# Performance work log

Measured on AMD Instinct MI355X. Metric: run time of the kernel, lower is better.

## Reference

```python
import jax, jax.numpy as jnp
import numpy as np

B = 32
IMG = 512
P = 32            # patch_size (must equal 32 so bounding_box Linear(32,4) type-checks)
G = IMG // P      # 16
N = G * G         # 256 num_patches
PD = P * P * 3    # 3072 patch_dim
D = 512           # project_dim
H = 8             # num_heads
DH = D // H
L = 4             # transformer blocks
HEAD_DIMS = [N * D, 2048, 1024, 512, 64, 32]
EPS = 1e-6


def _mk(key, shape, scale=0.02):
    return (jax.random.normal(key, shape, dtype=jnp.float32) * scale)


def setup_inputs() -> dict:
    key = jax.random.key(0)
    ks = jax.random.split(key, 32)
    inp = {"images": jax.random.normal(ks[0], (B, IMG, IMG, 3), dtype=jnp.float32)}
    # patch encoder
    inp["W_proj"] = _mk(ks[1], (PD, D))
    inp["b_proj"] = jnp.zeros((D,), jnp.float32)
    inp["pos_emb"] = _mk(ks[2], (N, D))
    # stacked transformer block params [L, ...]
    inp["ln1_g"] = jnp.ones((L, D), jnp.float32)
    inp["ln1_b"] = jnp.zeros((L, D), jnp.float32)
    inp["qkv_w"] = _mk(ks[3], (L, 3 * D, D))
    inp["qkv_b"] = jnp.zeros((L, 3 * D), jnp.float32)
    inp["attn_out_w"] = _mk(ks[4], (L, D, D))
    inp["attn_out_b"] = jnp.zeros((L, D), jnp.float32)
    inp["ln2_g"] = jnp.ones((L, D), jnp.float32)
    inp["ln2_b"] = jnp.zeros((L, D), jnp.float32)
    inp["mlp_w1"] = _mk(ks[5], (L, D, 2 * D))
    inp["mlp_b1"] = jnp.zeros((L, 2 * D), jnp.float32)
    inp["mlp_w2"] = _mk(ks[6], (L, 2 * D, D))
    inp["mlp_b2"] = jnp.zeros((L, D), jnp.float32)
    # final LN
    inp["lnf_g"] = jnp.ones((D,), jnp.float32)
    inp["lnf_b"] = jnp.zeros((D,), jnp.float32)
    # MLP head (5 layers) + bbox
    for i in range(5):
        inp[f"hW{i+1}"] = _mk(ks[7 + i], (HEAD_DIMS[i], HEAD_DIMS[i + 1]))
        inp[f"hb{i+1}"] = jnp.zeros((HEAD_DIMS[i + 1],), jnp.float32)
    inp["bbW"] = _mk(ks[20], (32, 4))
    inp["bbb"] = jnp.zeros((4,), jnp.float32)
    return inp


def _ln(x, g, b):
    m = jnp.mean(x, axis=-1, keepdims=True)
    v = jnp.mean((x - m) ** 2, axis=-1, keepdims=True)
    return (x - m) * jax.lax.rsqrt(v + EPS) * g + b


def _patches(images):
    # fused unfold: [B,IMG,IMG,3] -> [B,N,P*P*3], flatten order (ph, pw, c)
    x = images.reshape(B, G, P, G, P, 3)
    x = x.transpose(0, 1, 3, 2, 4, 5)  # [B,G,G,P,P,3]
    return x.reshape(B, N, PD)


def _block(x, ln1_g, ln1_b, qkv_w, qkv_b, out_w, out_b, ln2_g, ln2_b, w1, b1, w2, b2):
    x1 = _ln(x, ln1_g, ln1_b)
    qkv = x1 @ qkv_w.T + qkv_b  # [B,N,3D]
    q, k, v = jnp.split(qkv, 3, axis=-1)
    q = q.reshape(B, N, H, DH).transpose(0, 2, 1, 3)
    k = k.reshape(B, N, H, DH).transpose(0, 2, 1, 3)
    v = v.reshape(B, N, H, DH).transpose(0, 2, 1, 3)
    scores = jnp.einsum("bhqd,bhkd->bhqk", q, k) / jnp.sqrt(jnp.float32(DH))
    attn = jax.nn.softmax(scores, axis=-1)
    o = jnp.einsum("bhqk,bhkd->bhqd", attn, v)
    o = o.transpose(0, 2, 1, 3).reshape(B, N, D)
    attn_out = o @ out_w.T + out_b
    x2 = attn_out + x
    x3 = _ln(x2, ln2_g, ln2_b)
    h = jax.nn.gelu(x3 @ w1 + b1, approximate=False)
    h = jax.nn.gelu(h @ w2 + b2, approximate=False)
    return h + x2


def reference(images, W_proj, b_proj, pos_emb,
              ln1_g, ln1_b, qkv_w, qkv_b, attn_out_w, attn_out_b,
              ln2_g, ln2_b, mlp_w1, mlp_b1, mlp_w2, mlp_b2,
              lnf_g, lnf_b,
              hW1, hb1, hW2, hb2, hW3, hb3, hW4, hb4, hW5, hb5,
              bbW, bbb):
    patches = _patches(images)                       # [B,N,PD]
    x = patches @ W_proj + b_proj + pos_emb          # [B,N,D]
    for i in range(L):
        x = _block(x, ln1_g[i], ln1_b[i], qkv_w[i], qkv_b[i],
                   attn_out_w[i], attn_out_b[i], ln2_g[i], ln2_b[i],
                   mlp_w1[i], mlp_b1[i], mlp_w2[i], mlp_b2[i])
    rep = _ln(x, lnf_g, lnf_b).reshape(B, N * D)
    f = rep
    for (w, b) in [(hW1, hb1), (hW2, hb2), (hW3, hb3), (hW4, hb4), (hW5, hb5)]:
        f = jax.nn.gelu(f @ w + b, approximate=False)
    return f @ bbW + bbb                              # [B,4]
```

## Files before the change

kernel.cpp:

```cpp
#include <hip/hip_runtime.h>
#include <cstdint>
#include <cstddef>

#define DEV __device__ __forceinline__

typedef float f32x4 __attribute__((ext_vector_type(4)));
typedef short s16x8 __attribute__((ext_vector_type(8)));

DEV float gelu_f(float x) { return 0.5f * x * (1.0f + erff(x * 0.70710678118654752f)); }

DEV uint32_t fbits(float x) { return __builtin_bit_cast(uint32_t, x); }

DEV uint16_t bf16_rne(float x) {
    uint32_t u = fbits(x);
    return (uint16_t)((u + 0x7FFFu + ((u >> 16) & 1u)) >> 16);
}

DEV void gload16(const void* g, void* l) {
    __builtin_amdgcn_global_load_lds(
        (const __attribute__((address_space(1))) uint32_t*)g,
        (__attribute__((address_space(3))) uint32_t*)l, 16, 0, 0);
}

template<int BM, int BN, bool BIAS, bool GELU, bool RES, bool POS,
         bool OUTF32, bool OUTB16>
__global__ __launch_bounds__(256)
void mfma_gemm(const uint16_t* __restrict__ Ah, const uint16_t* __restrict__ Bh,
               float* __restrict__ C, uint16_t* __restrict__ Cb,
               const float* __restrict__ bias, const float* __restrict__ res,
               const float* __restrict__ pos, int M, int N, int K)
{
    constexpr int WTM = BM / 2, WTN = BN / 2;
    constexpr int FM = WTM / 16, FN = WTN / 16;
    constexpr int NA = BM / 16, NB = BN / 16;
    constexpr int TI = NA + NB;
    constexpr int TI4 = TI / 4;
    constexpr int HALF = (BM + BN) * 64;
    constexpr int BNP = BN + 4;
    constexpr int CR  = 32;
    constexpr int NCH = BM / CR;
    static_assert(CR * BNP * 4 <= 2 * HALF, "chunk must fit LDS");

    __shared__ __align__(16) uint8_t smem[2 * HALF];
    constexpr int offB = BM * 64;

    const int tid = threadIdx.x;
    const int w = tid >> 6, l = tid & 63;
    const int wr = w >> 1, wc = w & 1;

    const int gx = gridDim.x;
    const int nwg = gx * gridDim.y;
    const int lin = blockIdx.y * gx + blockIdx.x;
    const int cpx = nwg >> 3;
    const int swz = (lin & 7) * cpx + (lin >> 3);
    const int bxs = swz % gx, bys = swz / gx;
    const int bm0 = bys * BM, bn0 = bxs * BN;
    const size_t sK = (size_t)K * 2;

    const int srow  = l >> 2;
    const int sslot = (l & 3) ^ ((l >> 3) & 3);
    const uint8_t* gsrc[TI4];
    uint32_t loff[TI4];
#pragma unroll
    for (int j = 0; j < TI4; ++j) {
        int f = w * TI4 + j;
        int p = (f < NA) ? 0 : 1;
        int c = p ? (f - NA) : f;
        const uint16_t* base = p ? Bh : Ah;
        int rb = p ? bn0 : bm0;
        gsrc[j] = (const uint8_t*)base + (size_t)(rb + c * 16 + srow) * sK + sslot * 16;
        loff[j] = (uint32_t)((p ? offB : 0) + c * 1024);
    }

    const int lr = l & 15;
    const int sl16 = ((l >> 4) ^ ((lr >> 1) & 3)) * 16;
    const int aofs = (wr * WTM + lr) * 64 + sl16;
    const int bofs = (wc * WTN + lr) * 64 + sl16;

    f32x4 acc[FM][FN];
#pragma unroll
    for (int m = 0; m < FM; ++m)
#pragma unroll
        for (int n = 0; n < FN; ++n) acc[m][n] = (f32x4){0.f, 0.f, 0.f, 0.f};

    {
        const uint8_t* s0 = smem;
#pragma unroll
        for (int j = 0; j < TI4; ++j)
            gload16(gsrc[j], (void*)(s0 + loff[j]));
    }
    asm volatile("s_waitcnt vmcnt(0)" ::: "memory");
    __builtin_amdgcn_s_barrier();

    int cur = 0;
    for (int k0 = 0; k0 < K; k0 += 32) {
        const bool more = (k0 + 32 < K);
        if (more) {
            const size_t kb = (size_t)(k0 + 32) * 2;
            uint8_t* dst = smem + (cur ^ 1) * HALF;
#pragma unroll
            for (int j = 0; j < TI4; ++j)
                gload16(gsrc[j] + kb, dst + loff[j]);
        }
        const uint8_t* sb = smem + cur * HALF;
        s16x8 af[FM], bf[FN];
#pragma unroll
        for (int m = 0; m < FM; ++m)
            af[m] = *(const s16x8*)(sb + aofs + m * 1024);
#pragma unroll
        for (int n = 0; n < FN; ++n)
            bf[n] = *(const s16x8*)(sb + offB + bofs + n * 1024);
#pragma unroll
        for (int m = 0; m < FM; ++m)
#pragma unroll
            for (int n = 0; n < FN; ++n)
                acc[m][n] = __builtin_amdgcn_mfma_f32_16x16x32_bf16(af[m], bf[n], acc[m][n], 0, 0, 0);

        if (more) {
            asm volatile("s_waitcnt vmcnt(0)" ::: "memory");
            __builtin_amdgcn_s_barrier();
        }
        cur ^= 1;
    }

    float* lf = (float*)smem;
    const int r4 = (l >> 4) * 4;

    constexpr int C4PR = BN / 4;
    constexpr int RPP  = 256 / C4PR;
    const int rr = tid / C4PR, c4 = tid % C4PR;
    const int nn = bn0 + c4 * 4;

    float4 bv = {0.f, 0.f, 0.f, 0.f};
    if (BIAS) bv = *(const float4*)(bias + nn);

#pragma unroll
    for (int c = 0; c < NCH; ++c) {
        __syncthreads();
        if (wr == (c * CR) / WTM) {
            const int mlo = ((c * CR) % WTM) / 16;
#pragma unroll
            for (int mi = 0; mi < CR / 16; ++mi) {
                int m = mlo + mi;
#pragma unroll
                for (int n = 0; n < FN; ++n) {
                    int col = wc * WTN + n * 16 + lr;
#pragma unroll
                    for (int r = 0; r < 4; ++r) {
                        int lrow = mi * 16 + r4 + r;
                        lf[lrow * BNP + col] = acc[m][n][r];
                    }
                }
            }
        }
        __syncthreads();
#pragma unroll
        for (int p = 0; p < CR / RPP; ++p) {
            int row = p * RPP + rr;
            int mm = bm0 + c * CR + row;
            float4 v = *(const float4*)&lf[row * BNP + c4 * 4];
            float* vp = &v.x;
            const float* bp = &bv.x;
#pragma unroll
            for (int q = 0; q < 4; ++q) {
                float x = vp[q];
                if (BIAS) x += bp[q];
                if (GELU) x = gelu_f(x);
                vp[q] = x;
            }
            if (RES) {
                float4 rv = *(const float4*)(res + (size_t)mm * N + nn);
                v.x += rv.x; v.y += rv.y; v.z += rv.z; v.w += rv.w;
            }
            if (POS) {
                float4 pv = *(const float4*)(pos + (size_t)(mm & 255) * N + nn);
                v.x += pv.x; v.y += pv.y; v.z += pv.z; v.w += pv.w;
            }
            size_t o = (size_t)mm * N + nn;
            if (OUTF32) *(float4*)(C + o) = v;
            if (OUTB16) {
                ushort4 hh;
                hh.x = bf16_rne(v.x); hh.y = bf16_rne(v.y);
                hh.z = bf16_rne(v.z); hh.w = bf16_rne(v.w);
                *(ushort4*)(Cb + o) = hh;
            }
        }
    }
}

__global__ __launch_bounds__(256)
void mfma_attn(const uint16_t* __restrict__ QKVb, uint16_t* __restrict__ Oh)
{
    __shared__ __align__(16) uint8_t lds[55296];
    uint8_t* Ks = lds;
    uint8_t* Vt = lds + 9216;
    uint8_t* Ps = lds + 18432;

    const int tid = threadIdx.x;
    const int w = tid >> 6, l = tid & 63;
    const int lr = l & 15, lg = l >> 4;
    const int bh = blockIdx.x;
    const int b = bh >> 3, h = bh & 7;
    const uint16_t* base = QKVb + (size_t)b * 256 * 1536 + h * 64;
    const int q0 = w * 64;

    s16x8 qreg[2][4];
#pragma unroll
    for (int ks = 0; ks < 2; ++ks)
#pragma unroll
        for (int m = 0; m < 4; ++m)
            qreg[ks][m] = *(const s16x8*)(base + (size_t)(q0 + m * 16 + lr) * 1536 + ks * 32 + lg * 8);

    f32x4 oacc[4][4];
    float lrun[4][4];
#pragma unroll
    for (int m = 0; m < 4; ++m)
#pragma unroll
        for (int n = 0; n < 4; ++n) { oacc[m][n] = (f32x4){0.f,0.f,0.f,0.f}; lrun[m][n] = 0.f; }

    for (int kt = 0; kt < 4; ++kt) {
        __syncthreads();
        {
            int r = tid >> 2, sp = (tid & 3) * 2;
            const uint16_t* kp = base + (size_t)(kt * 64 + r) * 1536 + 512;
#pragma unroll
            for (int ss = 0; ss < 2; ++ss) {
                int s = sp + ss;
                *(s16x8*)(Ks + r * 144 + s * 16) = *(const s16x8*)(kp + s * 8);
            }
        }
        {
            int k = tid & 63, d0 = (tid >> 6) * 16;
            const uint16_t* vp = base + (size_t)(kt * 64 + k) * 1536 + 1024 + d0;
            s16x8 a = *(const s16x8*)(vp);
            s16x8 c = *(const s16x8*)(vp + 8);
#pragma unroll
            for (int i = 0; i < 8; ++i) {
                *(uint16_t*)(Vt + (d0 + i) * 144 + k * 2)     = (uint16_t)a[i];
                *(uint16_t*)(Vt + (d0 + 8 + i) * 144 + k * 2) = (uint16_t)c[i];
            }
        }
        __syncthreads();

        f32x4 sacc[4][4];
#pragma unroll
        for (int m = 0; m < 4; ++m)
#pragma unroll
            for (int n = 0; n < 4; ++n) sacc[m][n] = (f32x4){0.f,0.f,0.f,0.f};
#pragma unroll
        for (int ks = 0; ks < 2; ++ks) {
            s16x8 kf[4];
#pragma unroll
            for (int n = 0; n < 4; ++n)
                kf[n] = *(const s16x8*)(Ks + (n * 16 + lr) * 144 + ks * 64 + lg * 16);
#pragma unroll
            for (int m = 0; m < 4; ++m)
#pragma unroll
                for (int n = 0; n < 4; ++n)
                    sacc[m][n] = __builtin_amdgcn_mfma_f32_16x16x32_bf16(qreg[ks][m], kf[n], sacc[m][n], 0, 0, 0);
        }

        float dp[4][4];
#pragma unroll
        for (int m = 0; m < 4; ++m)
#pragma unroll
            for (int r = 0; r < 4; ++r) dp[m][r] = 0.f;
#pragma unroll
        for (int m = 0; m < 4; ++m) {
#pragma unroll
            for (int n = 0; n < 4; ++n) {
#pragma unroll
                for (int r = 0; r < 4; ++r) {
                    float e = __expf(sacc[m][n][r] * 0.125f);
                    dp[m][r] += e;
                    int q = q0 + m * 16 + lg * 4 + r;
                    int k = n * 16 + lr;
                    *(uint16_t*)(Ps + q * 144 + k * 2) = bf16_rne(e);
                }
            }
        }
#pragma unroll
        for (int m = 0; m < 4; ++m)
#pragma unroll
            for (int r = 0; r < 4; ++r) {
                float d = dp[m][r];
                d += __shfl_xor(d, 1);
                d += __shfl_xor(d, 2);
                d += __shfl_xor(d, 4);
                d += __shfl_xor(d, 8);
                lrun[m][r] += d;
            }

        asm volatile("s_waitcnt lgkmcnt(0)" ::: "memory");
        __builtin_amdgcn_sched_barrier(0);

#pragma unroll
        for (int ks = 0; ks < 2; ++ks) {
            s16x8 pf[4], vf[4];
#pragma unroll
            for (int m = 0; m < 4; ++m)
                pf[m] = *(const s16x8*)(Ps + (q0 + m * 16 + lr) * 144 + ks * 64 + lg * 16);
#pragma unroll
            for (int n = 0; n < 4; ++n)
                vf[n] = *(const s16x8*)(Vt + (n * 16 + lr) * 144 + ks * 64 + lg * 16);
#pragma unroll
            for (int m = 0; m < 4; ++m)
#pragma unroll
                for (int n = 0; n < 4; ++n)
                    oacc[m][n] = __builtin_amdgcn_mfma_f32_16x16x32_bf16(pf[m], vf[n], oacc[m][n], 0, 0, 0);
        }
    }

    float inv[4][4];
#pragma unroll
    for (int m = 0; m < 4; ++m)
#pragma unroll
        for (int r = 0; r < 4; ++r) inv[m][r] = 1.f / lrun[m][r];

    float* OL = (float*)lds;
#pragma unroll
    for (int c = 0; c < 2; ++c) {
        __syncthreads();
        if ((w >> 1) == c) {
            const int lq0 = q0 - c * 128;
#pragma unroll
            for (int m = 0; m < 4; ++m)
#pragma unroll
                for (int n = 0; n < 4; ++n)
#pragma unroll
                    for (int r = 0; r < 4; ++r) {
                        int lq = lq0 + m * 16 + lg * 4 + r;
                        int d = n * 16 + lr;
                        OL[lq * 68 + d] = oacc[m][n][r] * inv[m][r];
                    }
        }
        __syncthreads();
#pragma unroll
        for (int p = 0; p < 8; ++p) {
            int lq = p * 16 + (tid >> 4);
            int q = c * 128 + lq;
            int d4 = tid & 15;
            f32x4 v = *(const f32x4*)(OL + lq * 68 + d4 * 4);
            ushort4 hh;
            hh.x = bf16_rne(v[0]); hh.y = bf16_rne(v[1]);
            hh.z = bf16_rne(v[2]); hh.w = bf16_rne(v[3]);
            size_t o = (size_t)(b * 256 + q) * 512 + h * 64 + d4 * 4;
            *(ushort4*)(Oh + o) = hh;
        }
    }
}

__global__ __launch_bounds__(256)
void img2planes_kernel(const float* __restrict__ img, uint16_t* __restrict__ Ph)
{
    int idx = blockIdx.x * 256 + threadIdx.x;
    if (idx >= 8192 * 768) return;
    int m = idx / 768, q = idx - (idx / 768) * 768;
    int k = q * 4;
    int bb = m >> 8, n = m & 255;
    int ph = k / 96, rem = k - ph * 96;
    int prow = ((n >> 4) << 5) + ph;
    int pcol0 = (n & 15) << 5;
    const float* s = img + (((size_t)bb * 512 + prow) * 512 + pcol0) * 3 + rem;
    float4 v = *(const float4*)s;
    ushort4 hh;
    hh.x = bf16_rne(v.x); hh.y = bf16_rne(v.y);
    hh.z = bf16_rne(v.z); hh.w = bf16_rne(v.w);
    *(ushort4*)(Ph + (size_t)m * 3072 + k) = hh;
}

__global__ __launch_bounds__(256)
void conv_direct_kernel(const float* __restrict__ src, uint16_t* __restrict__ dh, int total4)
{
    int idx = blockIdx.x * 256 + threadIdx.x;
    if (idx >= total4) return;
    float4 v = *(const float4*)(src + (size_t)idx * 4);
    ushort4 hh;
    hh.x = bf16_rne(v.x); hh.y = bf16_rne(v.y);
    hh.z = bf16_rne(v.z); hh.w = bf16_rne(v.w);
    *(ushort4*)(dh + (size_t)idx * 4) = hh;
}

__global__ __launch_bounds__(256)
void conv_transpose_kernel(const float* __restrict__ src, uint16_t* __restrict__ dh,
                           int K, int N)
{
    __shared__ float t[32][33];
    int k0 = blockIdx.x * 32, n0 = blockIdx.y * 32;
    const float* s = src + (size_t)blockIdx.z * K * N;
    size_t dbase = (size_t)blockIdx.z * N * K;
    int tid = threadIdx.x;
    {
        int kk = tid / 8, n4 = tid % 8;
        float4 v = *(const float4*)(s + (size_t)(k0 + kk) * N + n0 + n4 * 4);
        t[kk][n4 * 4 + 0] = v.x; t[kk][n4 * 4 + 1] = v.y;
        t[kk][n4 * 4 + 2] = v.z; t[kk][n4 * 4 + 3] = v.w;
    }
    __syncthreads();
    int nn = tid / 8, k4 = tid % 8;
    ushort4 hh;
    hh.x = bf16_rne(t[k4 * 4 + 0][nn]);
    hh.y = bf16_rne(t[k4 * 4 + 1][nn]);
    hh.z = bf16_rne(t[k4 * 4 + 2][nn]);
    hh.w = bf16_rne(t[k4 * 4 + 3][nn]);
    *(ushort4*)(dh + dbase + (size_t)(n0 + nn) * K + k0 + k4 * 4) = hh;
}

template<bool PLANES>
__global__ __launch_bounds__(256)
void ln_kernel(const float* __restrict__ X, const float* __restrict__ g,
               const float* __restrict__ b, float* __restrict__ Y,
               uint16_t* __restrict__ Yh, int nrows)
{
    int wave = threadIdx.x >> 6;
    int lane = threadIdx.x & 63;
    int row = blockIdx.x * 4 + wave;
    if (row >= nrows) return;
    const float* x = X + (size_t)row * 512;
    float4 v0 = ((const float4*)x)[lane];
    float4 v1 = ((const float4*)x)[lane + 64];
    float s  = v0.x + v0.y + v0.z + v0.w + v1.x + v1.y + v1.z + v1.w;
    float sq = v0.x*v0.x + v0.y*v0.y + v0.z*v0.z + v0.w*v0.w
             + v1.x*v1.x + v1.y*v1.y + v1.z*v1.z + v1.w*v1.w;
#pragma unroll
    for (int off = 32; off > 0; off >>= 1) {
        s  += __shfl_down(s, off);
        sq += __shfl_down(sq, off);
    }
    s  = __shfl(s, 0);
    sq = __shfl(sq, 0);
    float mean = s * (1.f / 512.f);
    float var  = sq * (1.f / 512.f) - mean * mean;
    float rinv = rsqrtf(var + 1e-6f);
    float4 g0 = ((const float4*)g)[lane], g1 = ((const float4*)g)[lane + 64];
    float4 b0 = ((const float4*)b)[lane], b1 = ((const float4*)b)[lane + 64];
    float4 o0, o1;
    o0.x = (v0.x - mean) * rinv * g0.x + b0.x;
    o0.y = (v0.y - mean) * rinv * g0.y + b0.y;
    o0.z = (v0.z - mean) * rinv * g0.z + b0.z;
    o0.w = (v0.w - mean) * rinv * g0.w + b0.w;
    o1.x = (v1.x - mean) * rinv * g1.x + b1.x;
    o1.y = (v1.y - mean) * rinv * g1.y + b1.y;
    o1.z = (v1.z - mean) * rinv * g1.z + b1.z;
    o1.w = (v1.w - mean) * rinv * g1.w + b1.w;
    if (PLANES) {
        ushort4 hh0, hh1;
        hh0.x = bf16_rne(o0.x); hh0.y = bf16_rne(o0.y);
        hh0.z = bf16_rne(o0.z); hh0.w = bf16_rne(o0.w);
        hh1.x = bf16_rne(o1.x); hh1.y = bf16_rne(o1.y);
        hh1.z = bf16_rne(o1.z); hh1.w = bf16_rne(o1.w);
        size_t base = (size_t)row * 512;
        *(ushort4*)(Yh + base + lane * 4)       = hh0;
        *(ushort4*)(Yh + base + 256 + lane * 4) = hh1;
    } else {
        float* y = Y + (size_t)row * 512;
        ((float4*)y)[lane]      = o0;
        ((float4*)y)[lane + 64] = o1;
    }
}

template<int BM, int BN, int BK, int TM, int TN, bool SPLITK>
__global__ __launch_bounds__(256)
void gemm_kernel(const float* __restrict__ A, const float* __restrict__ B,
                 float* __restrict__ C, int M, int N, int K, int kchunk)
{
    constexpr int TX = BN / TN;
    constexpr int TY = BM / TM;
    static_assert(TX * TY == 256, "bad tile config");
    __shared__ float As[BK][BM + 4];
    __shared__ float Bs[BK][BN + 4];
    const int tid = threadIdx.x;
    const int tx  = tid % TX;
    const int ty  = tid / TX;
    const int bn0 = blockIdx.x * BN;
    const int bm0 = blockIdx.y * BM;
    int kstart = 0, kend = K;
    if (SPLITK) { kstart = blockIdx.z * kchunk; kend = kstart + kchunk; }
    float acc[TM][TN];
#pragma unroll
    for (int i = 0; i < TM; ++i)
#pragma unroll
        for (int j = 0; j < TN; ++j) acc[i][j] = 0.f;
    for (int k0 = kstart; k0 < kend; k0 += BK) {
        __syncthreads();
        constexpr int AV = BM * BK / 4 / 256;
#pragma unroll
        for (int r = 0; r < AV; ++r) {
            int idx = tid + r * 256;
            int k4 = idx % (BK / 4);
            int mm = idx / (BK / 4);
            float4 v = *(const float4*)(A + (size_t)(bm0 + mm) * K + k0 + k4 * 4);
            As[k4 * 4 + 0][mm] = v.x;
            As[k4 * 4 + 1][mm] = v.y;
            As[k4 * 4 + 2][mm] = v.z;
            As[k4 * 4 + 3][mm] = v.w;
        }
        constexpr int BV = BK * BN / 4 / 256;
#pragma unroll
        for (int r = 0; r < BV; ++r) {
            int idx = tid + r * 256;
            int n4 = idx % (BN / 4);
            int kk = idx / (BN / 4);
            float4 v = *(const float4*)(B + (size_t)(k0 + kk) * N + bn0 + n4 * 4);
            *(float4*)&Bs[kk][n4 * 4] = v;
        }
        __syncthreads();
#pragma unroll
        for (int kk = 0; kk < BK; ++kk) {
            float a[TM], b[TN];
#pragma unroll
            for (int i = 0; i < TM; i += 4)
                *(float4*)&a[i] = *(const float4*)&As[kk][ty * TM + i];
#pragma unroll
            for (int j = 0; j < TN; j += 4)
                *(float4*)&b[j] = *(const float4*)&Bs[kk][tx * TN + j];
#pragma unroll
            for (int i = 0; i < TM; ++i)
#pragma unroll
                for (int j = 0; j < TN; ++j)
                    acc[i][j] = fmaf(a[i], b[j], acc[i][j]);
        }
    }
    float* Cb = C;
    if (SPLITK) Cb += (size_t)blockIdx.z * M * N;
#pragma unroll
    for (int i = 0; i < TM; ++i) {
        int m = bm0 + ty * TM + i;
#pragma unroll
        for (int j = 0; j < TN; j += 4) {
            int n = bn0 + tx * TN + j;
            float4 v;
            v.x = acc[i][j + 0]; v.y = acc[i][j + 1];
            v.z = acc[i][j + 2]; v.w = acc[i][j + 3];
            *(float4*)(Cb + (size_t)m * N + n) = v;
        }
    }
}

__global__ __launch_bounds__(256)
void skinny_gemm_kernel(const float* __restrict__ A, const float* __restrict__ B,
                        float* __restrict__ P, int M, int N, int K, int kchunk)
{
    __shared__ float As[32][36];
    const int tid = threadIdx.x;
    const int tx  = tid & 63;
    const int ty  = tid >> 6;
    const int bn0 = blockIdx.x * 64;
    const int kstart = blockIdx.y * kchunk;
    const int kend   = kstart + kchunk;
    float acc[8];
#pragma unroll
    for (int i = 0; i < 8; ++i) acc[i] = 0.f;
    for (int k0 = kstart; k0 < kend; k0 += 32) {
        __syncthreads();
        {
            int row = tid >> 3;
            int k4  = tid & 7;
            float4 v = *(const float4*)(A + (size_t)row * K + k0 + k4 * 4);
            *(float4*)&As[row][k4 * 4] = v;
        }
        __syncthreads();
#pragma unroll 8
        for (int kk = 0; kk < 32; ++kk) {
            float b = B[(size_t)(k0 + kk) * N + bn0 + tx];
#pragma unroll
            for (int i = 0; i < 8; ++i)
                acc[i] = fmaf(As[ty * 8 + i][kk], b, acc[i]);
        }
    }
    float* Pb = P + (size_t)blockIdx.y * M * N;
#pragma unroll
    for (int i = 0; i < 8; ++i)
        Pb[(size_t)(ty * 8 + i) * N + bn0 + tx] = acc[i];
}

__global__ __launch_bounds__(256)
void reduce_gelu_kernel(const float* __restrict__ P, const float* __restrict__ bias,
                        float* __restrict__ Y, int total, int chunks, int N)
{
    int idx = blockIdx.x * 256 + threadIdx.x;
    if (idx >= total) return;
    float s = 0.f;
    for (int c = 0; c < chunks; ++c) s += P[(size_t)c * total + idx];
    s += bias[idx % N];
    Y[idx] = gelu_f(s);
}

template<bool GELU>
__global__ __launch_bounds__(256)
void small_gemm_kernel(const float* __restrict__ A, const float* __restrict__ B,
                       const float* __restrict__ bias, float* __restrict__ C,
                       int M, int N, int K)
{
    int idx = blockIdx.x * 256 + threadIdx.x;
    if (idx >= M * N) return;
    int m = idx / N, n = idx % N;
    const float* a = A + (size_t)m * K;
    float s = 0.f;
    for (int k = 0; k < K; ++k) s = fmaf(a[k], B[(size_t)k * N + n], s);
    s += bias[n];
    if (GELU) s = gelu_f(s);
    C[idx] = s;
}

extern "C" void kernel_launch(void* const* d_in, const int* in_sizes, int n_in,
                              void* d_out, int out_size, void* d_ws, size_t ws_size,
                              hipStream_t stream)
{
    const float* images     = (const float*)d_in[0];
    const float* W_proj     = (const float*)d_in[1];
    const float* b_proj     = (const float*)d_in[2];
    const float* pos_emb    = (const float*)d_in[3];
    const float* ln1_g      = (const float*)d_in[4];
    const float* ln1_b      = (const float*)d_in[5];
    const float* qkv_w      = (const float*)d_in[6];
    const float* qkv_b      = (const float*)d_in[7];
    const float* attn_out_w = (const float*)d_in[8];
    const float* attn_out_b = (const float*)d_in[9];
    const float* ln2_g      = (const float*)d_in[10];
    const float* ln2_b      = (const float*)d_in[11];
    const float* mlp_w1     = (const float*)d_in[12];
    const float* mlp_b1     = (const float*)d_in[13];
    const float* mlp_w2     = (const float*)d_in[14];
    const float* mlp_b2     = (const float*)d_in[15];
    const float* lnf_g      = (const float*)d_in[16];
    const float* lnf_b      = (const float*)d_in[17];
    const float* hW1 = (const float*)d_in[18];
    const float* hb1 = (const float*)d_in[19];
    const float* hW2 = (const float*)d_in[20];
    const float* hb2 = (const float*)d_in[21];
    const float* hW3 = (const float*)d_in[22];
    const float* hb3 = (const float*)d_in[23];
    const float* hW4 = (const float*)d_in[24];
    const float* hb4 = (const float*)d_in[25];
    const float* hW5 = (const float*)d_in[26];
    const float* hb5 = (const float*)d_in[27];
    const float* bbW = (const float*)d_in[28];
    const float* bbb = (const float*)d_in[29];

    uint8_t* wsb = (uint8_t*)d_ws;
    size_t off = 0;
    auto alloc = [&](size_t bytes) { uint8_t* p = wsb + off; off += (bytes + 255) & ~(size_t)255; return p; };
    float*    X    = (float*)alloc(8192ull * 512 * 4);
    uint16_t* QKVb = (uint16_t*)alloc(8192ull * 1536 * 2);
    float*    T    = (float*)alloc(8192ull * 512 * 4);
    uint16_t* Xh   = (uint16_t*)alloc(8192ull * 512 * 2);
    uint16_t* Ohp  = (uint16_t*)alloc(8192ull * 512 * 2);
    uint16_t* Hh   = (uint16_t*)alloc(8192ull * 1024 * 2);
    uint16_t* Ph   = (uint16_t*)alloc(8192ull * 3072 * 2);
    uint16_t* WqH  = (uint16_t*)alloc(4ull * 1536 * 512 * 2);
    uint16_t* WaH  = (uint16_t*)alloc(4ull * 512 * 512 * 2);
    uint16_t* WpH  = (uint16_t*)alloc(512ull * 3072 * 2);
    uint16_t* W1H  = (uint16_t*)alloc(4ull * 1024 * 512 * 2);
    uint16_t* W2H  = (uint16_t*)alloc(4ull * 512 * 1024 * 2);
    float*    F1p  = (float*)alloc(128ull * 65536 * 4);
    float*    F1   = (float*)alloc(65536ull * 4);
    float*    P2   = (float*)alloc(64ull * 32768 * 4);
    float*    F2   = (float*)alloc(32768ull * 4);
    float*    P3   = (float*)alloc(32ull * 16384 * 4);
    float*    F3   = (float*)alloc(16384ull * 4);
    float*    P4   = (float*)alloc(16ull * 2048 * 4);
    float*    F4   = (float*)alloc(2048ull * 4);
    float*    F5   = (float*)alloc(1024ull * 4);

    dim3 blk(256);

    img2planes_kernel<<<(8192 * 768 + 255) / 256, blk, 0, stream>>>(images, Ph);
    conv_direct_kernel<<<(4 * 1536 * 512 / 4 + 255) / 256, blk, 0, stream>>>(qkv_w, WqH, 4 * 1536 * 512 / 4);
    conv_direct_kernel<<<(4 * 512 * 512 / 4 + 255) / 256, blk, 0, stream>>>(attn_out_w, WaH, 4 * 512 * 512 / 4);
    conv_transpose_kernel<<<dim3(3072 / 32, 512 / 32, 1), blk, 0, stream>>>(W_proj, WpH, 3072, 512);
    conv_transpose_kernel<<<dim3(512 / 32, 1024 / 32, 4), blk, 0, stream>>>(mlp_w1, W1H, 512, 1024);
    conv_transpose_kernel<<<dim3(1024 / 32, 512 / 32, 4), blk, 0, stream>>>(mlp_w2, W2H, 1024, 512);

    mfma_gemm<64, 128, true, false, false, true, true, false>
        <<<dim3(512 / 128, 8192 / 64), blk, 0, stream>>>(
            Ph, WpH, X, nullptr, b_proj, nullptr, pos_emb, 8192, 512, 3072);

    for (int l = 0; l < 4; ++l) {
        ln_kernel<true><<<2048, blk, 0, stream>>>(X, ln1_g + l * 512, ln1_b + l * 512,
                                                  nullptr, Xh, 8192);
        mfma_gemm<128, 128, true, false, false, false, false, true>
            <<<dim3(1536 / 128, 8192 / 128), blk, 0, stream>>>(
                Xh, WqH + (size_t)l * 1536 * 512, nullptr, QKVb,
                qkv_b + l * 1536, nullptr, nullptr, 8192, 1536, 512);
        mfma_attn<<<256, blk, 0, stream>>>(QKVb, Ohp);
        mfma_gemm<64, 128, true, false, true, false, true, false>
            <<<dim3(512 / 128, 8192 / 64), blk, 0, stream>>>(
                Ohp, WaH + (size_t)l * 512 * 512, X, nullptr,
                attn_out_b + l * 512, X, nullptr, 8192, 512, 512);
        ln_kernel<true><<<2048, blk, 0, stream>>>(X, ln2_g + l * 512, ln2_b + l * 512,
                                                  nullptr, Xh, 8192);
        mfma_gemm<128, 128, true, true, false, false, false, true>
            <<<dim3(1024 / 128, 8192 / 128), blk, 0, stream>>>(
                Xh, W1H + (size_t)l * 1024 * 512, nullptr, Hh,
                mlp_b1 + l * 1024, nullptr, nullptr, 8192, 1024, 512);
        mfma_gemm<64, 128, true, true, true, false, true, false>
            <<<dim3(512 / 128, 8192 / 64), blk, 0, stream>>>(
                Hh, W2H + (size_t)l * 512 * 1024, X, nullptr,
                mlp_b2 + l * 512, X, nullptr, 8192, 512, 1024);
    }

    ln_kernel<false><<<2048, blk, 0, stream>>>(X, lnf_g, lnf_b, T, nullptr, 8192);

    gemm_kernel<32, 128, 32, 4, 4, true>
        <<<dim3(2048 / 128, 1, 128), blk, 0, stream>>>(
            T, hW1, F1p, 32, 2048, 131072, 131072 / 128);
    reduce_gelu_kernel<<<(65536 + 255) / 256, blk, 0, stream>>>(F1p, hb1, F1, 65536, 128, 2048);

    skinny_gemm_kernel<<<dim3(1024 / 64, 2048 / 32), blk, 0, stream>>>(F1, hW2, P2, 32, 1024, 2048, 32);
    reduce_gelu_kernel<<<(32768 + 255) / 256, blk, 0, stream>>>(P2, hb2, F2, 32768, 64, 1024);

    skinny_gemm_kernel<<<dim3(512 / 64, 1024 / 32), blk, 0, stream>>>(F2, hW3, P3, 32, 512, 1024, 32);
    reduce_gelu_kernel<<<(16384 + 255) / 256, blk, 0, stream>>>(P3, hb3, F3, 16384, 32, 512);

    skinny_gemm_kernel<<<dim3(64 / 64, 512 / 32), blk, 0, stream>>>(F3, hW4, P4, 32, 64, 512, 32);
    reduce_gelu_kernel<<<(2048 + 255) / 256, blk, 0, stream>>>(P4, hb4, F4, 2048, 16, 64);

    small_gemm_kernel<true><<<(32 * 32 + 255) / 256, blk, 0, stream>>>(F4, hW5, hb5, F5, 32, 32, 64);
    small_gemm_kernel<false><<<1, blk, 0, stream>>>(F5, bbW, bbb, (float*)d_out, 32, 4, 32);
}
```

Baseline: 1.053 ms.

## Triple-buffer MFMA GEMM k-loop and fuse small head/conversion kernels

The MFMA GEMM moves from double to triple buffering in LDS. Loads are issued two k-steps ahead and waited on with a partial vmcnt, so global-to-LDS latency is hidden better. The two weight-conversion launches are merged into one, and the last head layers (hW4, hW5, bbox) are fused into a single one-block kernel, which removes several tiny launches. In exchange, LDS use grows by half, which can lower occupancy, and the fused tail runs on a single workgroup.

```diff
diff --git a/kernel.cpp b/kernel.cpp
--- a/kernel.cpp
+++ b/kernel.cpp
@@ -20,6 +20,16 @@
     __builtin_amdgcn_global_load_lds(
         (const __attribute__((address_space(1))) uint32_t*)g,
         (__attribute__((address_space(3))) uint32_t*)l, 16, 0, 0);
+}
+
+template<int N>
+DEV void waitcnt_vm() {
+    if constexpr (N == 0)      asm volatile("s_waitcnt vmcnt(0)" ::: "memory");
+    else if constexpr (N == 2) asm volatile("s_waitcnt vmcnt(2)" ::: "memory");
+    else if constexpr (N == 3) asm volatile("s_waitcnt vmcnt(3)" ::: "memory");
+    else if constexpr (N == 4) asm volatile("s_waitcnt vmcnt(4)" ::: "memory");
+    else if constexpr (N == 6) asm volatile("s_waitcnt vmcnt(6)" ::: "memory");
+    else static_assert(N == 0, "unsupported vmcnt");
 }
 
 template<int BM, int BN, bool BIAS, bool GELU, bool RES, bool POS,
@@ -39,9 +49,9 @@
     constexpr int BNP = BN + 4;
     constexpr int CR  = 32;
     constexpr int NCH = BM / CR;
-    static_assert(CR * BNP * 4 <= 2 * HALF, "chunk must fit LDS");
-
-    __shared__ __align__(16) uint8_t smem[2 * HALF];
+    static_assert(CR * BNP * 4 <= 3 * HALF, "chunk must fit LDS");
+
+    __shared__ __align__(16) uint8_t smem[3 * HALF];
     constexpr int offB = BM * 64;
 
     const int tid = threadIdx.x;
@@ -83,26 +93,25 @@
 #pragma unroll
         for (int n = 0; n < FN; ++n) acc[m][n] = (f32x4){0.f, 0.f, 0.f, 0.f};
 
-    {
-        const uint8_t* s0 = smem;
-#pragma unroll
-        for (int j = 0; j < TI4; ++j)
-            gload16(gsrc[j], (void*)(s0 + loff[j]));
-    }
-    asm volatile("s_waitcnt vmcnt(0)" ::: "memory");
+    const int NT = K >> 5;
+#pragma unroll
+    for (int j = 0; j < TI4; ++j)
+        gload16(gsrc[j], smem + loff[j]);
+#pragma unroll
+    for (int j = 0; j < TI4; ++j)
+        gload16(gsrc[j] + 64, smem + HALF + loff[j]);
+    waitcnt_vm<TI4>();
     __builtin_amdgcn_s_barrier();
 
-    int cur = 0;
-    for (int k0 = 0; k0 < K; k0 += 32) {
-        const bool more = (k0 + 32 < K);
-        if (more) {
-            const size_t kb = (size_t)(k0 + 32) * 2;
-            uint8_t* dst = smem + (cur ^ 1) * HALF;
+    for (int t = 0; t < NT; ++t) {
+        if (t + 2 < NT) {
+            const size_t kb = (size_t)(t + 2) * 64;
+            uint8_t* dst = smem + ((t + 2) % 3) * HALF;
 #pragma unroll
             for (int j = 0; j < TI4; ++j)
                 gload16(gsrc[j] + kb, dst + loff[j]);
         }
-        const uint8_t* sb = smem + cur * HALF;
+        const uint8_t* sb = smem + (t % 3) * HALF;
         s16x8 af[FM], bf[FN];
 #pragma unroll
         for (int m = 0; m < FM; ++m)
@@ -116,11 +125,13 @@
             for (int n = 0; n < FN; ++n)
                 acc[m][n] = __builtin_amdgcn_mfma_f32_16x16x32_bf16(af[m], bf[n], acc[m][n], 0, 0, 0);
 
-        if (more) {
-            asm volatile("s_waitcnt vmcnt(0)" ::: "memory");
+        if (t + 2 < NT) {
+            waitcnt_vm<TI4>();
             __builtin_amdgcn_s_barrier();
-        }
-        cur ^= 1;
+        } else if (t + 1 < NT) {
+            waitcnt_vm<0>();
+            __builtin_amdgcn_s_barrier();
+        }
     }
 
     float* lf = (float*)smem;
@@ -370,15 +381,19 @@
 }
 
 __global__ __launch_bounds__(256)
-void conv_direct_kernel(const float* __restrict__ src, uint16_t* __restrict__ dh, int total4)
+void conv_direct2_kernel(const float* __restrict__ s1, uint16_t* __restrict__ d1, int n1,
+                         const float* __restrict__ s2, uint16_t* __restrict__ d2, int n2)
 {
     int idx = blockIdx.x * 256 + threadIdx.x;
-    if (idx >= total4) return;
-    float4 v = *(const float4*)(src + (size_t)idx * 4);
+    const float* s; uint16_t* d; int i;
+    if (idx < n1) { s = s1; d = d1; i = idx; }
+    else if (idx < n1 + n2) { s = s2; d = d2; i = idx - n1; }
+    else return;
+    float4 v = *(const float4*)(s + (size_t)i * 4);
     ushort4 hh;
     hh.x = bf16_rne(v.x); hh.y = bf16_rne(v.y);
     hh.z = bf16_rne(v.z); hh.w = bf16_rne(v.w);
-    *(ushort4*)(dh + (size_t)idx * 4) = hh;
+    *(ushort4*)(d + (size_t)i * 4) = hh;
 }
 
 __global__ __launch_bounds__(256)
@@ -586,21 +601,57 @@
     Y[idx] = gelu_f(s);
 }
 
-template<bool GELU>
-__global__ __launch_bounds__(256)
-void small_gemm_kernel(const float* __restrict__ A, const float* __restrict__ B,
-                       const float* __restrict__ bias, float* __restrict__ C,
-                       int M, int N, int K)
-{
-    int idx = blockIdx.x * 256 + threadIdx.x;
-    if (idx >= M * N) return;
-    int m = idx / N, n = idx % N;
-    const float* a = A + (size_t)m * K;
-    float s = 0.f;
-    for (int k = 0; k < K; ++k) s = fmaf(a[k], B[(size_t)k * N + n], s);
-    s += bias[n];
-    if (GELU) s = gelu_f(s);
-    C[idx] = s;
+__global__ __launch_bounds__(256)
+void head_tail_kernel(const float* __restrict__ F3, const float* __restrict__ hW4,
+                      const float* __restrict__ hb4, const float* __restrict__ hW5,
+                      const float* __restrict__ hb5, const float* __restrict__ bbW,
+                      const float* __restrict__ bbb, float* __restrict__ out)
+{
+    __shared__ float F4s[32 * 64];
+    __shared__ float F5s[32 * 32];
+    const int tid = threadIdx.x;
+
+    {
+        const int n = tid & 63, mw = tid >> 6;
+        float acc[8];
+#pragma unroll
+        for (int i = 0; i < 8; ++i) acc[i] = 0.f;
+        for (int k = 0; k < 512; ++k) {
+            float wv = hW4[(size_t)k * 64 + n];
+#pragma unroll
+            for (int i = 0; i < 8; ++i)
+                acc[i] = fmaf(F3[(size_t)(i * 4 + mw) * 512 + k], wv, acc[i]);
+        }
+#pragma unroll
+        for (int i = 0; i < 8; ++i)
+            F4s[(i * 4 + mw) * 64 + n] = gelu_f(acc[i] + hb4[n]);
+    }
+    __syncthreads();
+
+    {
+        const int n = tid & 31, mw = tid >> 5;
+        float acc[4];
+#pragma unroll
+        for (int i = 0; i < 4; ++i) acc[i] = 0.f;
+        for (int k = 0; k < 64; ++k) {
+            float wv = hW5[(size_t)k * 32 + n];
+#pragma unroll
+            for (int i = 0; i < 4; ++i)
+                acc[i] = fmaf(F4s[(i * 8 + mw) * 64 + k], wv, acc[i]);
+        }
+#pragma unroll
+        for (int i = 0; i < 4; ++i)
+            F5s[(i * 8 + mw) * 32 + n] = gelu_f(acc[i] + hb5[n]);
+    }
+    __syncthreads();
+
+    if (tid < 128) {
+        int m = tid >> 2, n = tid & 3;
+        float s = 0.f;
+        for (int k = 0; k < 32; ++k)
+            s = fmaf(F5s[m * 32 + k], bbW[(size_t)k * 4 + n], s);
+        out[m * 4 + n] = s + bbb[n];
+    }
 }
 
 extern "C" void kernel_launch(void* const* d_in, const int* in_sizes, int n_in,
@@ -659,15 +710,12 @@
     float*    F2   = (float*)alloc(32768ull * 4);
     float*    P3   = (float*)alloc(32ull * 16384 * 4);
     float*    F3   = (float*)alloc(16384ull * 4);
-    float*    P4   = (float*)alloc(16ull * 2048 * 4);
-    float*    F4   = (float*)alloc(2048ull * 4);
-    float*    F5   = (float*)alloc(1024ull * 4);
 
     dim3 blk(256);
 
     img2planes_kernel<<<(8192 * 768 + 255) / 256, blk, 0, stream>>>(images, Ph);
-    conv_direct_kernel<<<(4 * 1536 * 512 / 4 + 255) / 256, blk, 0, stream>>>(qkv_w, WqH, 4 * 1536 * 512 / 4);
-    conv_direct_kernel<<<(4 * 512 * 512 / 4 + 255) / 256, blk, 0, stream>>>(attn_out_w, WaH, 4 * 512 * 512 / 4);
+    conv_direct2_kernel<<<(1048576 + 255) / 256, blk, 0, stream>>>(
+        qkv_w, WqH, 786432, attn_out_w, WaH, 262144);
     conv_transpose_kernel<<<dim3(3072 / 32, 512 / 32, 1), blk, 0, stream>>>(W_proj, WpH, 3072, 512);
     conv_transpose_kernel<<<dim3(512 / 32, 1024 / 32, 4), blk, 0, stream>>>(mlp_w1, W1H, 512, 1024);
     conv_transpose_kernel<<<dim3(1024 / 32, 512 / 32, 4), blk, 0, stream>>>(mlp_w2, W2H, 1024, 512);
@@ -713,9 +761,5 @@
     skinny_gemm_kernel<<<dim3(512 / 64, 1024 / 32), blk, 0, stream>>>(F2, hW3, P3, 32, 512, 1024, 32);
     reduce_gelu_kernel<<<(16384 + 255) / 256, blk, 0, stream>>>(P3, hb3, F3, 16384, 32, 512);
 
-    skinny_gemm_kernel<<<dim3(64 / 64, 512 / 32), blk, 0, stream>>>(F3, hW4, P4, 32, 64, 512, 32);
-    reduce_gelu_kernel<<<(2048 + 255) / 256, blk, 0, stream>>>(P4, hb4, F4, 2048, 16, 64);
-
-    small_gemm_kernel<true><<<(32 * 32 + 255) / 256, blk, 0, stream>>>(F4, hW5, hb5, F5, 32, 32, 64);
-    small_gemm_kernel<false><<<1, blk, 0, stream>>>(F5, bbW, bbb, (float*)d_out, 32, 4, 32);
-}
+    head_tail_kernel<<<1, blk, 0, stream>>>(F3, hW4, hb4, hW5, hb5, bbW, bbb, (float*)d_out);
+}
```

After: 995.8 us, median of 2. 5.4% less time.
